# Kernel tuning notes

Hardware: AMD Instinct MI355X
Metric: run time of the kernel (lower is better)

Reference implementation:

```python
import jax, jax.numpy as jnp
import numpy as np

D_MODEL = 256
NUM_HEADS = 8
HEAD_DIM = D_MODEL // NUM_HEADS
SCALE = HEAD_DIM ** -0.5
LN_EPS = 1e-5


def setup_inputs() -> dict:
    key = jax.random.key(0)
    ks = jax.random.split(key, 16)
    B, N, H, W = 1, 8, 16, 16
    s = 1.0 / np.sqrt(D_MODEL)
    inp = {
        'features': jax.random.normal(ks[0], (B, N, H, W, D_MODEL), jnp.float32),
        'pointmaps': jax.random.normal(ks[1], (B, N, H, W, 3), jnp.float32),
        'Wq': jax.random.normal(ks[2], (D_MODEL, D_MODEL), jnp.float32) * s,
        'bq': jnp.zeros((D_MODEL,), jnp.float32),
        'Wk': jax.random.normal(ks[3], (D_MODEL, D_MODEL), jnp.float32) * s,
        'bk': jnp.zeros((D_MODEL,), jnp.float32),
        'Wv': jax.random.normal(ks[4], (D_MODEL, D_MODEL), jnp.float32) * s,
        'bv': jnp.zeros((D_MODEL,), jnp.float32),
        'Wo': jax.random.normal(ks[5], (D_MODEL, D_MODEL), jnp.float32) * s,
        'bo': jnp.zeros((D_MODEL,), jnp.float32),
        'beta': jnp.asarray(1.0, jnp.float32),
        'k_w1': jax.random.normal(ks[6], (32, 1), jnp.float32) * 0.1,
        'k_b1': jnp.zeros((32,), jnp.float32),
        'k_w2': jax.random.normal(ks[7], (1, 32), jnp.float32) * 0.1,
        'k_b2': jnp.full((1,), -1.0, jnp.float32),
        'ln_g': jnp.ones((D_MODEL,), jnp.float32),
        'ln_b': jnp.zeros((D_MODEL,), jnp.float32),
    }
    return inp


def _gasa_forward(features, pointmaps, Wq, bq, Wk, bk, Wv, bv, Wo, bo,
                  beta, k_w1, k_b1, k_w2, k_b2, ln_g, ln_b):
    B, N, H, W, D = features.shape
    L = N * H * W
    x = features.reshape(B, L, D)

    # QKV projections (torch Linear: x @ W.T + b)
    Q = (x @ Wq.T + bq).reshape(B, L, NUM_HEADS, HEAD_DIM).transpose(0, 2, 1, 3)
    K = (x @ Wk.T + bk).reshape(B, L, NUM_HEADS, HEAD_DIM).transpose(0, 2, 1, 3)
    V = (x @ Wv.T + bv).reshape(B, L, NUM_HEADS, HEAD_DIM).transpose(0, 2, 1, 3)

    # semantic scores [B, h, L, L]
    scores = jnp.einsum('bhqd,bhkd->bhqk', Q, K) * SCALE

    # geometric bias: pairwise 3D distances + tiny MLP kernel, clamp to [-10, 0]
    pts = pointmaps.reshape(B, L, 3)
    diff = pts[:, :, None, :] - pts[:, None, :, :]           # [B, L, L, 3]
    sq = jnp.sum(diff * diff, axis=-1)                        # [B, L, L]
    dist = jnp.where(sq > 0, jnp.sqrt(jnp.where(sq > 0, sq, 1.0)), 0.0)
    h = jax.nn.relu(dist[..., None] * k_w1[:, 0] + k_b1)      # [B, L, L, 32]
    bias = h @ k_w2[0] + k_b2[0]                              # [B, L, L]
    bias = jnp.clip(bias, -10.0, 0.0)

    scores = scores + beta * bias[:, None, :, :]
    probs = jax.nn.softmax(scores, axis=-1)
    out = jnp.einsum('bhqk,bhkd->bhqd', probs, V)
    out = out.transpose(0, 2, 1, 3).reshape(B, L, D)
    out = out @ Wo.T + bo

    # residual + LayerNorm
    y = x + out
    mu = jnp.mean(y, axis=-1, keepdims=True)
    var = jnp.mean(jnp.square(y - mu), axis=-1, keepdims=True)
    y = (y - mu) * jax.lax.rsqrt(var + LN_EPS) * ln_g + ln_b
    return y.reshape(B, N, H, W, D)


def reference(features, pointmaps, Wq, bq, Wk, bk, Wv, bv, Wo, bo,
              beta, k_w1, k_b1, k_w2, k_b2, ln_g, ln_b):
    return _gasa_forward(features, pointmaps, Wq, bq, Wk, bk, Wv, bv, Wo, bo,
                         beta, k_w1, k_b1, k_w2, k_b2, ln_g, ln_b)
```

## Files before the change

### kernel.cpp

```cpp
#include <hip/hip_runtime.h>
#include <math.h>

#define L_SEQ 2048
#define DM    256
#define NH    8
#define HD    32

typedef __attribute__((ext_vector_type(8))) short bf16x8;
typedef __attribute__((ext_vector_type(4))) float f32x4;

__device__ __forceinline__ unsigned short f2bf(float f) {
    unsigned int u = __builtin_bit_cast(unsigned int, f);
    u += 0x7fff + ((u >> 16) & 1);
    return (unsigned short)(u >> 16);
}

__global__ __launch_bounds__(256) void prep(
    const float* __restrict__ x,  const float* __restrict__ wq,
    const float* __restrict__ wk, const float* __restrict__ wv,
    const float* __restrict__ wo,
    const float* __restrict__ k_w1, const float* __restrict__ k_b1,
    const float* __restrict__ k_w2, const float* __restrict__ k_b2,
    const float* __restrict__ beta_p,
    unsigned short* __restrict__ xb,  unsigned short* __restrict__ wqb,
    unsigned short* __restrict__ wkb, unsigned short* __restrict__ wvb,
    unsigned short* __restrict__ wob, float* __restrict__ T)
{
    const int bx = blockIdx.x, t = threadIdx.x;
    if (bx < 384) {
        int e = (bx * 256 + t) * 8;
        const float* src; unsigned short* dst; int off;
        if      (e < 524288) { src = x;  dst = xb;  off = e; }
        else if (e < 589824) { src = wq; dst = wqb; off = e - 524288; }
        else if (e < 655360) { src = wk; dst = wkb; off = e - 589824; }
        else if (e < 720896) { src = wv; dst = wvb; off = e - 655360; }
        else                 { src = wo; dst = wob; off = e - 720896; }
        float4 u = *(const float4*)(src + off);
        float4 v = *(const float4*)(src + off + 4);
        ushort4 a, b;
        a.x = f2bf(u.x); a.y = f2bf(u.y); a.z = f2bf(u.z); a.w = f2bf(u.w);
        b.x = f2bf(v.x); b.y = f2bf(v.y); b.z = f2bf(v.z); b.w = f2bf(v.w);
        *(ushort4*)(dst + off)     = a;
        *(ushort4*)(dst + off + 4) = b;
    } else {
        int n = (bx - 384) * 256 + t;
        float d = (float)n * (1.0f / 256.0f);
        float s = 0.f;
#pragma unroll
        for (int k = 0; k < 32; ++k)
            s += fmaxf(fmaf(d, k_w1[k], k_b1[k]), 0.f) * k_w2[k];
        s = fminf(fmaxf(s + k_b2[0], -10.f), 0.f);
        T[n] = beta_p[0] * s;
    }
}

__global__ __launch_bounds__(256) void fused_front(
    const unsigned short* __restrict__ xb, const float* __restrict__ pts,
    const unsigned short* __restrict__ wqb, const float* __restrict__ bq,
    const unsigned short* __restrict__ wkb, const float* __restrict__ bk,
    const unsigned short* __restrict__ wvb, const float* __restrict__ bv,
    const float* __restrict__ T,
    unsigned short* __restrict__ Qb, unsigned short* __restrict__ Kb,
    unsigned short* __restrict__ Vt, unsigned short* __restrict__ biasP)
{
    const int bx = blockIdx.x;
    const int t = threadIdx.x;

    if (bx < 384) {
        const int z  = bx >> 7;
        const int r0 = (bx & 127) << 4;
        const int w = t >> 6, lane = t & 63, quad = lane >> 4, c = lane & 15;
        const int c0 = w * 64;
        const unsigned short* Wm = (z == 0) ? wqb : (z == 1) ? wkb : wvb;
        const float* bia         = (z == 0) ? bq  : (z == 1) ? bk  : bv;

        f32x4 acc[4] = {};
        for (int kt = 0; kt < 8; ++kt) {
            bf16x8 a = *(const bf16x8*)(xb + (size_t)(r0 + c) * DM + kt * 32 + quad * 8);
#pragma unroll
            for (int ct = 0; ct < 4; ++ct) {
                bf16x8 b = *(const bf16x8*)(Wm + (size_t)(c0 + ct * 16 + c) * DM + kt * 32 + quad * 8);
                acc[ct] = __builtin_amdgcn_mfma_f32_16x16x32_bf16(a, b, acc[ct], 0, 0, 0);
            }
        }
        if (z < 2) {
            unsigned short* out = (z == 0) ? Qb : Kb;
#pragma unroll
            for (int ct = 0; ct < 4; ++ct) {
                float bc = bia[c0 + ct * 16 + c];
#pragma unroll
                for (int reg = 0; reg < 4; ++reg) {
                    int r = r0 + quad * 4 + reg;
                    out[(size_t)r * DM + c0 + ct * 16 + c] = f2bf(acc[ct][reg] + bc);
                }
            }
        } else {
#pragma unroll
            for (int ct = 0; ct < 4; ++ct) {
                int col = c0 + ct * 16 + c;
                float bc = bia[col];
#pragma unroll
                for (int reg = 0; reg < 4; ++reg) {
                    int key = r0 + quad * 4 + reg;
                    int loc = key & 31;
                    int pos = (key & ~31) + 2 * (loc & 15) + (loc >> 4);
                    Vt[(size_t)col * L_SEQ + pos] = f2bf(acc[ct][reg] + bc);
                }
            }
        }
    } else {
        const int b = bx - 384;
        const int i = b >> 1;
        const int p0 = ((b & 1) * 256 + t) * 4;
        const float xi = pts[i * 3], yi = pts[i * 3 + 1], zi = pts[i * 3 + 2];

        ushort4 o; unsigned short* po = (unsigned short*)&o;
#pragma unroll
        for (int v = 0; v < 4; ++v) {
            int p = p0 + v, loc = p & 31, base = p & ~31;
            int k = base + (loc >> 1) + 16 * (loc & 1);
            float dx = xi - pts[k * 3], dy = yi - pts[k * 3 + 1], dz = zi - pts[k * 3 + 2];
            float dist = sqrtf(dx * dx + dy * dy + dz * dz);
            float fn = dist * 256.0f;
            int n = (int)fn; n = (n > 4094) ? 4094 : n;
            float fr = fn - (float)n;
            float t0 = T[n], t1 = T[n + 1];
            po[v] = f2bf(fmaf(fr, t1 - t0, t0));
        }
        *(ushort4*)(biasP + (size_t)i * L_SEQ + p0) = o;
    }
}

__global__ __launch_bounds__(256) void attn_mfma(
    const unsigned short* __restrict__ Qb, const unsigned short* __restrict__ Kb,
    const unsigned short* __restrict__ Vt, const unsigned short* __restrict__ biasP,
    unsigned short* __restrict__ Ab)
{
    __shared__ unsigned short Plds[4][32][40];
    __shared__ float Ol[4][32][36];
    __shared__ float Ll[4][32];
    const int t = threadIdx.x, w = t >> 6, lane = t & 63, quad = lane >> 4, c = lane & 15;
    const int h = blockIdx.y, r0 = blockIdx.x * 32;
    const int kbase = w * 512;
    const f32x4 Z = {};

    bf16x8 qf0 = *(const bf16x8*)(Qb + (size_t)(r0 + c) * DM + h * HD + quad * 8);
    bf16x8 qf1 = *(const bf16x8*)(Qb + (size_t)(r0 + 16 + c) * DM + h * HD + quad * 8);

    f32x4 O00 = {}, O01 = {}, O10 = {}, O11 = {};
    float l0[4] = {0.f,0.f,0.f,0.f}, l1[4] = {0.f,0.f,0.f,0.f};

    const float LOG2E = 1.4426950408889634f;
    const float C1 = 0.17677669529663687f * LOG2E;
    const float MC = -10.0f * LOG2E;

    const unsigned short* Kp  = Kb + (size_t)h * HD + quad * 8;
    const unsigned short* Vp0 = Vt + (size_t)(h * HD + c) * L_SEQ + quad * 8;
    const unsigned short* Vp1 = Vt + (size_t)(h * HD + 16 + c) * L_SEQ + quad * 8;
    const int br0 = r0 + quad * 4;

    bf16x8 kf0 = *(const bf16x8*)(Kp + (size_t)(kbase + c) * DM);
    bf16x8 kf1 = *(const bf16x8*)(Kp + (size_t)(kbase + 16 + c) * DM);
    bf16x8 vf0 = *(const bf16x8*)(Vp0 + kbase);
    bf16x8 vf1 = *(const bf16x8*)(Vp1 + kbase);
    unsigned int bu0[4], bu1[4];
#pragma unroll
    for (int reg = 0; reg < 4; ++reg) {
        bu0[reg] = *(const unsigned int*)(biasP + (size_t)(br0 + reg) * L_SEQ + kbase + c * 2);
        bu1[reg] = *(const unsigned int*)(biasP + (size_t)(br0 + 16 + reg) * L_SEQ + kbase + c * 2);
    }

    for (int kt = 0; kt < 16; ++kt) {
        const int kn = kbase + (kt + 1) * 32;
        bf16x8 nk0 = kf0, nk1 = kf1, nv0 = vf0, nv1 = vf1;
        unsigned int nbu0[4], nbu1[4];
#pragma unroll
        for (int reg = 0; reg < 4; ++reg) { nbu0[reg] = bu0[reg]; nbu1[reg] = bu1[reg]; }
        if (kt < 15) {
            nk0 = *(const bf16x8*)(Kp + (size_t)(kn + c) * DM);
            nk1 = *(const bf16x8*)(Kp + (size_t)(kn + 16 + c) * DM);
            nv0 = *(const bf16x8*)(Vp0 + kn);
            nv1 = *(const bf16x8*)(Vp1 + kn);
#pragma unroll
            for (int reg = 0; reg < 4; ++reg) {
                nbu0[reg] = *(const unsigned int*)(biasP + (size_t)(br0 + reg) * L_SEQ + kn + c * 2);
                nbu1[reg] = *(const unsigned int*)(biasP + (size_t)(br0 + 16 + reg) * L_SEQ + kn + c * 2);
            }
        }

        f32x4 S00 = __builtin_amdgcn_mfma_f32_16x16x32_bf16(qf0, kf0, Z, 0, 0, 0);
        f32x4 S01 = __builtin_amdgcn_mfma_f32_16x16x32_bf16(qf0, kf1, Z, 0, 0, 0);
        f32x4 S10 = __builtin_amdgcn_mfma_f32_16x16x32_bf16(qf1, kf0, Z, 0, 0, 0);
        f32x4 S11 = __builtin_amdgcn_mfma_f32_16x16x32_bf16(qf1, kf1, Z, 0, 0, 0);

#pragma unroll
        for (int reg = 0; reg < 4; ++reg) {
            unsigned int u = bu0[reg];
            float blo = __builtin_bit_cast(float, u << 16);
            float bhi = __builtin_bit_cast(float, u & 0xffff0000u);
            float p0 = __builtin_exp2f(fmaf(S00[reg], C1, fmaf(blo, LOG2E, MC)));
            float p1 = __builtin_exp2f(fmaf(S01[reg], C1, fmaf(bhi, LOG2E, MC)));
            l0[reg] += p0 + p1;
            unsigned int pb = __builtin_amdgcn_perm(
                __builtin_bit_cast(unsigned int, p1),
                __builtin_bit_cast(unsigned int, p0), 0x07060302);
            *(unsigned int*)&Plds[w][quad * 4 + reg][c * 2] = pb;

            u = bu1[reg];
            blo = __builtin_bit_cast(float, u << 16);
            bhi = __builtin_bit_cast(float, u & 0xffff0000u);
            p0 = __builtin_exp2f(fmaf(S10[reg], C1, fmaf(blo, LOG2E, MC)));
            p1 = __builtin_exp2f(fmaf(S11[reg], C1, fmaf(bhi, LOG2E, MC)));
            l1[reg] += p0 + p1;
            pb = __builtin_amdgcn_perm(
                __builtin_bit_cast(unsigned int, p1),
                __builtin_bit_cast(unsigned int, p0), 0x07060302);
            *(unsigned int*)&Plds[w][16 + quad * 4 + reg][c * 2] = pb;
        }

        bf16x8 pa0 = *(const bf16x8*)&Plds[w][c][quad * 8];
        bf16x8 pa1 = *(const bf16x8*)&Plds[w][16 + c][quad * 8];
        O00 = __builtin_amdgcn_mfma_f32_16x16x32_bf16(pa0, vf0, O00, 0, 0, 0);
        O01 = __builtin_amdgcn_mfma_f32_16x16x32_bf16(pa0, vf1, O01, 0, 0, 0);
        O10 = __builtin_amdgcn_mfma_f32_16x16x32_bf16(pa1, vf0, O10, 0, 0, 0);
        O11 = __builtin_amdgcn_mfma_f32_16x16x32_bf16(pa1, vf1, O11, 0, 0, 0);

        kf0 = nk0; kf1 = nk1; vf0 = nv0; vf1 = nv1;
#pragma unroll
        for (int reg = 0; reg < 4; ++reg) { bu0[reg] = nbu0[reg]; bu1[reg] = nbu1[reg]; }
    }

#pragma unroll
    for (int off = 1; off < 16; off <<= 1) {
#pragma unroll
        for (int reg = 0; reg < 4; ++reg) {
            l0[reg] += __shfl_xor(l0[reg], off, 16);
            l1[reg] += __shfl_xor(l1[reg], off, 16);
        }
    }
#pragma unroll
    for (int reg = 0; reg < 4; ++reg) {
        int row = quad * 4 + reg;
        Ol[w][row][c]           = O00[reg];
        Ol[w][row][16 + c]      = O01[reg];
        Ol[w][row + 16][c]      = O10[reg];
        Ol[w][row + 16][16 + c] = O11[reg];
    }
    if (c == 0) {
#pragma unroll
        for (int reg = 0; reg < 4; ++reg) {
            Ll[w][quad * 4 + reg]      = l0[reg];
            Ll[w][quad * 4 + reg + 16] = l1[reg];
        }
    }
    __syncthreads();
    {
        int row = t >> 3, c4 = (t & 7) * 4;
        float4 a = *(const float4*)&Ol[0][row][c4];
        float4 b = *(const float4*)&Ol[1][row][c4];
        float4 d = *(const float4*)&Ol[2][row][c4];
        float4 e = *(const float4*)&Ol[3][row][c4];
        float inv = 1.0f / (Ll[0][row] + Ll[1][row] + Ll[2][row] + Ll[3][row]);
        ushort4 ob;
        ob.x = f2bf((a.x + b.x + d.x + e.x) * inv);
        ob.y = f2bf((a.y + b.y + d.y + e.y) * inv);
        ob.z = f2bf((a.z + b.z + d.z + e.z) * inv);
        ob.w = f2bf((a.w + b.w + d.w + e.w) * inv);
        *(ushort4*)(Ab + (size_t)(r0 + row) * DM + h * HD + c4) = ob;
    }
}

__global__ __launch_bounds__(256) void proj_ln(
    const unsigned short* __restrict__ Ab, const unsigned short* __restrict__ Wob,
    const float* __restrict__ bo, const float* __restrict__ feat,
    const float* __restrict__ ln_g, const float* __restrict__ ln_b,
    float* __restrict__ out)
{
    __shared__ float red1[4][16], red2[4][16];
    const int t = threadIdx.x, w = t >> 6, lane = t & 63, quad = lane >> 4, c = lane & 15;
    const int r0 = blockIdx.x * 16, c0 = w * 64;

    f32x4 acc[4] = {};
    for (int kt = 0; kt < 8; ++kt) {
        bf16x8 a = *(const bf16x8*)(Ab + (size_t)(r0 + c) * DM + kt * 32 + quad * 8);
#pragma unroll
        for (int ct = 0; ct < 4; ++ct) {
            bf16x8 b = *(const bf16x8*)(Wob + (size_t)(c0 + ct * 16 + c) * DM + kt * 32 + quad * 8);
            acc[ct] = __builtin_amdgcn_mfma_f32_16x16x32_bf16(a, b, acc[ct], 0, 0, 0);
        }
    }
    float y[4][4];
    float s1[4] = {0.f,0.f,0.f,0.f}, s2[4] = {0.f,0.f,0.f,0.f};
#pragma unroll
    for (int ct = 0; ct < 4; ++ct) {
        int col = c0 + ct * 16 + c;
        float bc = bo[col];
#pragma unroll
        for (int reg = 0; reg < 4; ++reg) {
            int r = r0 + quad * 4 + reg;
            float v = acc[ct][reg] + bc + feat[(size_t)r * DM + col];
            y[ct][reg] = v;
            s1[reg] += v; s2[reg] += v * v;
        }
    }
#pragma unroll
    for (int off = 1; off < 16; off <<= 1)
#pragma unroll
        for (int reg = 0; reg < 4; ++reg) {
            s1[reg] += __shfl_xor(s1[reg], off, 16);
            s2[reg] += __shfl_xor(s2[reg], off, 16);
        }
    if (c == 0)
#pragma unroll
        for (int reg = 0; reg < 4; ++reg) {
            red1[w][quad * 4 + reg] = s1[reg];
            red2[w][quad * 4 + reg] = s2[reg];
        }
    __syncthreads();
    float mu[4], rs[4];
#pragma unroll
    for (int reg = 0; reg < 4; ++reg) {
        int row = quad * 4 + reg;
        float a1 = red1[0][row] + red1[1][row] + red1[2][row] + red1[3][row];
        float a2 = red2[0][row] + red2[1][row] + red2[2][row] + red2[3][row];
        float m = a1 * (1.0f / 256.0f);
        mu[reg] = m;
        rs[reg] = rsqrtf(a2 * (1.0f / 256.0f) - m * m + 1e-5f);
    }
#pragma unroll
    for (int ct = 0; ct < 4; ++ct) {
        int col = c0 + ct * 16 + c;
        float g = ln_g[col], bb = ln_b[col];
#pragma unroll
        for (int reg = 0; reg < 4; ++reg) {
            int r = r0 + quad * 4 + reg;
            out[(size_t)r * DM + col] = (y[ct][reg] - mu[reg]) * rs[reg] * g + bb;
        }
    }
}

extern "C" void kernel_launch(void* const* d_in, const int* in_sizes, int n_in,
                              void* d_out, int out_size, void* d_ws, size_t ws_size,
                              hipStream_t stream) {
    (void)in_sizes; (void)n_in; (void)out_size; (void)ws_size;
    const float* features  = (const float*)d_in[0];
    const float* pointmaps = (const float*)d_in[1];
    const float* Wq = (const float*)d_in[2];  const float* bq = (const float*)d_in[3];
    const float* Wk = (const float*)d_in[4];  const float* bk = (const float*)d_in[5];
    const float* Wv = (const float*)d_in[6];  const float* bv = (const float*)d_in[7];
    const float* Wo = (const float*)d_in[8];  const float* bo = (const float*)d_in[9];
    const float* beta = (const float*)d_in[10];
    const float* k_w1 = (const float*)d_in[11]; const float* k_b1 = (const float*)d_in[12];
    const float* k_w2 = (const float*)d_in[13]; const float* k_b2 = (const float*)d_in[14];
    const float* ln_g = (const float*)d_in[15]; const float* ln_b = (const float*)d_in[16];
    float* out = (float*)d_out;

    char* W = (char*)d_ws;
    unsigned short* xb    = (unsigned short*)(W);
    unsigned short* Wqb   = (unsigned short*)(W + 1048576);
    unsigned short* Wkb   = (unsigned short*)(W + 1179648);
    unsigned short* Wvb   = (unsigned short*)(W + 1310720);
    unsigned short* Wob   = (unsigned short*)(W + 1441792);
    float*          T     = (float*)        (W + 1572864);
    unsigned short* Qb    = (unsigned short*)(W + 1589248);
    unsigned short* Kb    = (unsigned short*)(W + 2637824);
    unsigned short* Vt    = (unsigned short*)(W + 3686400);
    unsigned short* Ab    = (unsigned short*)(W + 4734976);
    unsigned short* biasP = (unsigned short*)(W + 5783552);

    prep       <<<400, 256, 0, stream>>>(features, Wq, Wk, Wv, Wo,
                                         k_w1, k_b1, k_w2, k_b2, beta,
                                         xb, Wqb, Wkb, Wvb, Wob, T);
    fused_front<<<4480, 256, 0, stream>>>(xb, pointmaps,
                                          Wqb, bq, Wkb, bk, Wvb, bv, T,
                                          Qb, Kb, Vt, biasP);
    attn_mfma  <<<dim3(64, 8), 256, 0, stream>>>(Qb, Kb, Vt, biasP, Ab);
    proj_ln    <<<128,         256, 0, stream>>>(Ab, Wob, bo, features, ln_g, ln_b, out);
}
```

Measured before the change: 136.8 us.

## Double waves per block in attention and quadruple waves in projection+LN

The attention kernel now uses 8 waves per block, each covering 256 keys instead of 512, and the cross-wave reduction of partial O and row sums is widened to 8 slices. The projection+LayerNorm kernel uses 16 waves with one 16-column tile each instead of 4 waves with four tiles each, and its LN reduction is reorganised across 16 waves. The aim is more in-flight waves per CU on a small grid (512 and 128 blocks), which should hide memory latency better. The cost is more LDS, a larger reduction per block, and more redundant A-fragment loads in the projection.

```diff
diff --git a/kernel.cpp b/kernel.cpp
--- a/kernel.cpp
+++ b/kernel.cpp
@@ -131,17 +131,17 @@
     }
 }
 
-__global__ __launch_bounds__(256) void attn_mfma(
+__global__ __launch_bounds__(512, 4) void attn_mfma(
     const unsigned short* __restrict__ Qb, const unsigned short* __restrict__ Kb,
     const unsigned short* __restrict__ Vt, const unsigned short* __restrict__ biasP,
     unsigned short* __restrict__ Ab)
 {
-    __shared__ unsigned short Plds[4][32][40];
-    __shared__ float Ol[4][32][36];
-    __shared__ float Ll[4][32];
+    __shared__ unsigned short Plds[8][32][40];
+    __shared__ float Ol[8][32][36];
+    __shared__ float Ll[8][32];
     const int t = threadIdx.x, w = t >> 6, lane = t & 63, quad = lane >> 4, c = lane & 15;
     const int h = blockIdx.y, r0 = blockIdx.x * 32;
-    const int kbase = w * 512;
+    const int kbase = w * 256;
     const f32x4 Z = {};
 
     bf16x8 qf0 = *(const bf16x8*)(Qb + (size_t)(r0 + c) * DM + h * HD + quad * 8);
@@ -170,13 +170,13 @@
         bu1[reg] = *(const unsigned int*)(biasP + (size_t)(br0 + 16 + reg) * L_SEQ + kbase + c * 2);
     }
 
-    for (int kt = 0; kt < 16; ++kt) {
+    for (int kt = 0; kt < 8; ++kt) {
         const int kn = kbase + (kt + 1) * 32;
         bf16x8 nk0 = kf0, nk1 = kf1, nv0 = vf0, nv1 = vf1;
         unsigned int nbu0[4], nbu1[4];
 #pragma unroll
         for (int reg = 0; reg < 4; ++reg) { nbu0[reg] = bu0[reg]; nbu1[reg] = bu1[reg]; }
-        if (kt < 15) {
+        if (kt < 7) {
             nk0 = *(const bf16x8*)(Kp + (size_t)(kn + c) * DM);
             nk1 = *(const bf16x8*)(Kp + (size_t)(kn + 16 + c) * DM);
             nv0 = *(const bf16x8*)(Vp0 + kn);
@@ -255,53 +255,47 @@
     }
     __syncthreads();
     {
-        int row = t >> 3, c4 = (t & 7) * 4;
-        float4 a = *(const float4*)&Ol[0][row][c4];
-        float4 b = *(const float4*)&Ol[1][row][c4];
-        float4 d = *(const float4*)&Ol[2][row][c4];
-        float4 e = *(const float4*)&Ol[3][row][c4];
-        float inv = 1.0f / (Ll[0][row] + Ll[1][row] + Ll[2][row] + Ll[3][row]);
-        ushort4 ob;
-        ob.x = f2bf((a.x + b.x + d.x + e.x) * inv);
-        ob.y = f2bf((a.y + b.y + d.y + e.y) * inv);
-        ob.z = f2bf((a.z + b.z + d.z + e.z) * inv);
-        ob.w = f2bf((a.w + b.w + d.w + e.w) * inv);
-        *(ushort4*)(Ab + (size_t)(r0 + row) * DM + h * HD + c4) = ob;
-    }
-}
-
-__global__ __launch_bounds__(256) void proj_ln(
+        int row = t >> 4, cc = (t & 15) * 2;
+        float a0 = 0.f, a1 = 0.f, lt = 0.f;
+#pragma unroll
+        for (int wv = 0; wv < 8; ++wv) {
+            a0 += Ol[wv][row][cc];
+            a1 += Ol[wv][row][cc + 1];
+            lt += Ll[wv][row];
+        }
+        float inv = 1.0f / lt;
+        ushort2 ob;
+        ob.x = f2bf(a0 * inv);
+        ob.y = f2bf(a1 * inv);
+        *(ushort2*)(Ab + (size_t)(r0 + row) * DM + h * HD + cc) = ob;
+    }
+}
+
+__global__ __launch_bounds__(1024, 4) void proj_ln(
     const unsigned short* __restrict__ Ab, const unsigned short* __restrict__ Wob,
     const float* __restrict__ bo, const float* __restrict__ feat,
     const float* __restrict__ ln_g, const float* __restrict__ ln_b,
     float* __restrict__ out)
 {
-    __shared__ float red1[4][16], red2[4][16];
+    __shared__ float red1[16][16], red2[16][16];
     const int t = threadIdx.x, w = t >> 6, lane = t & 63, quad = lane >> 4, c = lane & 15;
-    const int r0 = blockIdx.x * 16, c0 = w * 64;
-
-    f32x4 acc[4] = {};
+    const int r0 = blockIdx.x * 16, c0 = w * 16;
+
+    f32x4 acc = {};
     for (int kt = 0; kt < 8; ++kt) {
         bf16x8 a = *(const bf16x8*)(Ab + (size_t)(r0 + c) * DM + kt * 32 + quad * 8);
-#pragma unroll
-        for (int ct = 0; ct < 4; ++ct) {
-            bf16x8 b = *(const bf16x8*)(Wob + (size_t)(c0 + ct * 16 + c) * DM + kt * 32 + quad * 8);
-            acc[ct] = __builtin_amdgcn_mfma_f32_16x16x32_bf16(a, b, acc[ct], 0, 0, 0);
-        }
-    }
-    float y[4][4];
-    float s1[4] = {0.f,0.f,0.f,0.f}, s2[4] = {0.f,0.f,0.f,0.f};
-#pragma unroll
-    for (int ct = 0; ct < 4; ++ct) {
-        int col = c0 + ct * 16 + c;
-        float bc = bo[col];
-#pragma unroll
-        for (int reg = 0; reg < 4; ++reg) {
-            int r = r0 + quad * 4 + reg;
-            float v = acc[ct][reg] + bc + feat[(size_t)r * DM + col];
-            y[ct][reg] = v;
-            s1[reg] += v; s2[reg] += v * v;
-        }
+        bf16x8 b = *(const bf16x8*)(Wob + (size_t)(c0 + c) * DM + kt * 32 + quad * 8);
+        acc = __builtin_amdgcn_mfma_f32_16x16x32_bf16(a, b, acc, 0, 0, 0);
+    }
+    const int col = c0 + c;
+    const float bc = bo[col];
+    float y[4], s1[4], s2[4];
+#pragma unroll
+    for (int reg = 0; reg < 4; ++reg) {
+        int r = r0 + quad * 4 + reg;
+        float v = acc[reg] + bc + feat[(size_t)r * DM + col];
+        y[reg] = v;
+        s1[reg] = v; s2[reg] = v * v;
     }
 #pragma unroll
     for (int off = 1; off < 16; off <<= 1)
@@ -313,29 +307,25 @@
     if (c == 0)
 #pragma unroll
         for (int reg = 0; reg < 4; ++reg) {
-            red1[w][quad * 4 + reg] = s1[reg];
-            red2[w][quad * 4 + reg] = s2[reg];
+            red1[quad * 4 + reg][w] = s1[reg];
+            red2[quad * 4 + reg][w] = s2[reg];
         }
     __syncthreads();
-    float mu[4], rs[4];
+    const float g = ln_g[col], bb = ln_b[col];
 #pragma unroll
     for (int reg = 0; reg < 4; ++reg) {
         int row = quad * 4 + reg;
-        float a1 = red1[0][row] + red1[1][row] + red1[2][row] + red1[3][row];
-        float a2 = red2[0][row] + red2[1][row] + red2[2][row] + red2[3][row];
+        float a1 = 0.f, a2 = 0.f;
+        const float4* p1 = (const float4*)red1[row];
+        const float4* p2 = (const float4*)red2[row];
+#pragma unroll
+        for (int q4 = 0; q4 < 4; ++q4) {
+            float4 u = p1[q4]; a1 += u.x + u.y + u.z + u.w;
+            float4 v = p2[q4]; a2 += v.x + v.y + v.z + v.w;
+        }
         float m = a1 * (1.0f / 256.0f);
-        mu[reg] = m;
-        rs[reg] = rsqrtf(a2 * (1.0f / 256.0f) - m * m + 1e-5f);
-    }
-#pragma unroll
-    for (int ct = 0; ct < 4; ++ct) {
-        int col = c0 + ct * 16 + c;
-        float g = ln_g[col], bb = ln_b[col];
-#pragma unroll
-        for (int reg = 0; reg < 4; ++reg) {
-            int r = r0 + quad * 4 + reg;
-            out[(size_t)r * DM + col] = (y[ct][reg] - mu[reg]) * rs[reg] * g + bb;
-        }
+        float rsv = rsqrtf(a2 * (1.0f / 256.0f) - m * m + 1e-5f);
+        out[(size_t)(r0 + row) * DM + col] = (y[reg] - m) * rsv * g + bb;
     }
 }
 
@@ -374,6 +364,6 @@
     fused_front<<<4480, 256, 0, stream>>>(xb, pointmaps,
                                           Wqb, bq, Wkb, bk, Wvb, bv, T,
                                           Qb, Kb, Vt, biasP);
-    attn_mfma  <<<dim3(64, 8), 256, 0, stream>>>(Qb, Kb, Vt, biasP, Ab);
-    proj_ln    <<<128,         256, 0, stream>>>(Ab, Wob, bo, features, ln_g, ln_b, out);
-}
+    attn_mfma  <<<dim3(64, 8), 512, 0, stream>>>(Qb, Kb, Vt, biasP, Ab);
+    proj_ln    <<<128,        1024, 0, stream>>>(Ab, Wob, bo, features, ln_g, ln_b, out);
+}
```

Measured after the change: 141.7 us. 3.6% more time.
